# Kernel tuning notes

Measured on AMD Instinct MI355X. Metric: run time of the kernel, lower is better.

Reference implementation:

```python
import math
import jax, jax.numpy as jnp
import numpy as np

B, C_IN, H, W = 16, 384, 64, 64
CDIM, K, NSCALES, ITERS = 128, 64, 2, 3

def conv1x1(x, w, b):
    # x: [B,C,H,W], w: [O,C], b: [O]
    return jnp.einsum('bchw,oc->bohw', x, w) + b[None, :, None, None]

def mlp2(x, w1, b1, w2, b2):
    return conv1x1(jax.nn.relu(conv1x1(x, w1, b1)), w2, b2)

def log_optimal_transport(scores, dustbin, iters):
    B_, K_, N_ = scores.shape
    Z = jnp.concatenate([scores, dustbin], axis=1)  # [B,K+1,N]
    log_mu = jnp.full((B_, K_ + 1), -math.log(K_ + 1), dtype=scores.dtype)
    log_nu = jnp.full((B_, N_), -math.log(N_), dtype=scores.dtype)
    u = jnp.zeros_like(log_mu)
    v = jnp.zeros_like(log_nu)
    for _ in range(iters):
        u = log_mu - jax.nn.logsumexp(Z + v[:, None, :], axis=2)
        v = log_nu - jax.nn.logsumexp(Z + u[:, :, None], axis=1)
    return Z + u[:, :, None] + v[:, None, :]

def avg_pool2(x):
    b, c, h, w = x.shape
    return x.reshape(b, c, h // 2, 2, w // 2, 2).mean(axis=(3, 5))

def scale_branch(xs, fw1, fb1, fw2, fb2, sw1, sb1, sw2, sb2, dw1, db1, dw2, db2):
    b = xs.shape[0]
    local_feat = mlp2(xs, fw1, fb1, fw2, fb2).reshape(b, CDIM, -1)   # [B,C,N]
    score = mlp2(xs, sw1, sb1, sw2, sb2).reshape(b, K, -1)           # [B,K,N]
    dustbin = mlp2(xs, dw1, db1, dw2, db2).reshape(b, 1, -1)         # [B,1,N]
    log_p = log_optimal_transport(score, dustbin, ITERS)
    p = jnp.exp(log_p)[:, :-1, :]                                    # drop dustbin row
    p = p / (p.sum(axis=-1, keepdims=True) + 1e-8)
    out = jnp.einsum('bcn,bkn->bck', local_feat, p)                  # [B,C,K]
    out = out / jnp.clip(jnp.linalg.norm(out, axis=1, keepdims=True), 1e-12)
    return out.reshape(b, -1), local_feat

def setup_inputs():
    key = jax.random.key(0)
    ks = jax.random.split(key, 13)
    inp = {'x': jax.random.normal(ks[0], (B, C_IN, H, W), jnp.float32)}
    kidx = 1
    for s in range(NSCALES):
        for name, (o, i) in [('fw1', (512, C_IN)), ('fw2', (CDIM, 512)),
                              ('sw1', (512, C_IN)), ('sw2', (K, 512)),
                              ('dw1', (128, C_IN)), ('dw2', (1, 128))]:
            inp[f'{name}_{s}'] = 0.02 * jax.random.normal(ks[kidx % 13], (o, i), jnp.float32)
            inp[f'{name[0]}b{name[2]}_{s}'] = jnp.zeros((o,), jnp.float32)
            kidx += 1
    return inp

def reference(x,
              fw1_0, fb1_0, fw2_0, fb2_0, sw1_0, sb1_0, sw2_0, sb2_0, dw1_0, db1_0, dw2_0, db2_0,
              fw1_1, fb1_1, fw2_1, fb2_1, sw1_1, sb1_1, sw2_1, sb2_1, dw1_1, db1_1, dw2_1, db2_1):
    params = [
        (fw1_0, fb1_0, fw2_0, fb2_0, sw1_0, sb1_0, sw2_0, sb2_0, dw1_0, db1_0, dw2_0, db2_0),
        (fw1_1, fb1_1, fw2_1, fb2_1, sw1_1, sb1_1, sw2_1, sb2_1, dw1_1, db1_1, dw2_1, db2_1),
    ]
    descs = []
    xs = x
    for s in range(NSCALES):
        if s > 0:
            xs = avg_pool2(xs)
        d, _ = scale_branch(xs, *params[s])
        descs.append(d)
    g = jnp.stack(descs, axis=1).mean(axis=1)
    g = g / jnp.clip(jnp.linalg.norm(g, axis=1, keepdims=True), 1e-12)
    return g
```

## Files before the change

kernel.cpp:

```cpp
#include <hip/hip_runtime.h>
#include <math.h>

typedef __attribute__((ext_vector_type(8))) short short8;
typedef __attribute__((ext_vector_type(4))) float floatx4;

__device__ inline float bf2f(short s) {
    union { unsigned u; float f; } x; x.u = ((unsigned)(unsigned short)s) << 16; return x.f;
}
__device__ inline short f2bf(float f) {
    union { float f; unsigned u; } x; x.f = f;
    unsigned r = x.u + 0x7fff + ((x.u >> 16) & 1);
    return (short)(r >> 16);
}

struct WSet {
    const float *fw1, *fb1, *fw2, *sw1, *sb1, *sw2, *sb2, *dw1, *db1, *dw2, *db2;
};

__global__ __launch_bounds__(256) void wprep(WSet a0, WSet a1,
    short* __restrict__ W1f, short* __restrict__ W2af, short* __restrict__ W2bf,
    float* __restrict__ B1p, float* __restrict__ B2bp)
{
    const int s = blockIdx.y;
    const WSet A = s ? a1 : a0;
    W1f  += (size_t)s * 491520;
    W2af += (size_t)s * 65536;
    W2bf += (size_t)s * 98304;
    B1p  += s * 1280;
    B2bp += s * 128;
    int id = blockIdx.x * 256 + threadIdx.x;
    if (id < 491520) {
        int e = id & 7, l = (id >> 3) & 63, g = (id >> 9) & 15, rest = id >> 13;
        int kc = rest % 12, c = rest / 12;
        int m = c * 256 + g * 16 + (l & 15);
        int k = kc * 32 + (l >> 4) * 8 + e;
        float v = 0.f;
        if (m < 512) v = A.fw1[m * 384 + k];
        else if (m < 1024) v = A.sw1[(m - 512) * 384 + k];
        else if (m < 1152) v = A.dw1[(m - 1024) * 384 + k];
        W1f[id] = f2bf(v);
        return;
    }
    id -= 491520;
    if (id < 65536) {
        int e = id & 7, l = (id >> 3) & 63, g = (id >> 9) & 7, ka = id >> 12;
        int r = g * 16 + (l & 15), k = ka * 32 + (l >> 4) * 8 + e;
        W2af[id] = f2bf(A.fw2[r * 512 + k]);
        return;
    }
    id -= 65536;
    if (id < 98304) {
        int e = id & 7, l = (id >> 3) & 63, g = (id >> 9) & 7, kb = id >> 12;
        int r = g * 16 + (l & 15), krel = kb * 32 + (l >> 4) * 8 + e;
        float v = 0.f;
        if (r < 64 && krel < 512) v = A.sw2[r * 512 + krel];
        else if (r == 64 && krel >= 512 && krel < 640) v = A.dw2[krel - 512];
        W2bf[id] = f2bf(v);
        return;
    }
    id -= 98304;
    if (id < 1280) {
        float v = 0.f;
        if (id < 512) v = A.fb1[id];
        else if (id < 1024) v = A.sb1[id - 512];
        else if (id < 1152) v = A.db1[id - 1024];
        B1p[id] = v;
        return;
    }
    id -= 1280;
    if (id < 128) B2bp[id] = id < 64 ? A.sb2[id] : id == 64 ? A.db2[0] : 0.f;
}

__global__ __launch_bounds__(256) void xprep(const float* __restrict__ x,
                                             short* __restrict__ xT, short* __restrict__ x1T)
{
    __shared__ float xt[64 * 129];
    const int ip = blockIdx.x;
    const int cg = blockIdx.y;
    const int b  = blockIdx.z;
    const int t  = threadIdx.x;
    #pragma unroll
    for (int u = 0; u < 8; u++) {
        int idx = t + 256 * u;
        int c = idx >> 5, spq = idx & 31;
        float4 v = *(const float4*)&x[(((long)b * 384 + cg * 64 + c) * 64 + ip * 2 + (spq >> 4)) * 64 + (spq & 15) * 4];
        float* d = &xt[c * 129 + spq * 4];
        d[0] = v.x; d[1] = v.y; d[2] = v.z; d[3] = v.w;
    }
    __syncthreads();
    {
        int sp = t >> 1, ch = t & 1;
        short tmp[32];
        #pragma unroll
        for (int cc = 0; cc < 32; cc++) tmp[cc] = f2bf(xt[(ch * 32 + cc) * 129 + sp]);
        short* dst = xT + ((long)b * 4096 + ip * 128 + sp) * 384 + cg * 64 + ch * 32;
        #pragma unroll
        for (int v = 0; v < 4; v++) *(short8*)(dst + v * 8) = *(short8*)(tmp + v * 8);
    }
    {
        int j1 = t >> 3, c8 = t & 7;
        short tmp[8];
        #pragma unroll
        for (int e = 0; e < 8; e++) {
            int c = c8 * 8 + e;
            float v = 0.25f * (xt[c * 129 + j1 * 2]      + xt[c * 129 + j1 * 2 + 1] +
                               xt[c * 129 + 64 + j1 * 2] + xt[c * 129 + 64 + j1 * 2 + 1]);
            tmp[e] = f2bf(v);
        }
        *(short8*)(x1T + ((long)b * 1024 + ip * 32 + j1) * 384 + cg * 64 + c8 * 8) = *(short8*)tmp;
    }
}

__global__ __launch_bounds__(512, 4) void fused_mlp(
    const short* __restrict__ W1f_, const float* __restrict__ B1p_,
    const short* __restrict__ W2af_, const float* __restrict__ fb2_0, const float* __restrict__ fb2_1,
    const short* __restrict__ W2bf_, const float* __restrict__ B2bp_,
    const short* __restrict__ xT, const short* __restrict__ x1T,
    float* __restrict__ feat0, float* __restrict__ feat1,
    short* __restrict__ Eg0, short* __restrict__ Eg1,
    float* __restrict__ pu0, float* __restrict__ pu1)
{
    __shared__ short xs[12 * 2048];
    __shared__ short hs[8 * 2048];
    const int tid = threadIdx.x;
    const int wid = tid >> 6, lane = tid & 63;
    const int l15 = lane & 15, q = lane >> 4;
    const int bx = blockIdx.x, b = blockIdx.y;
    const int sc = bx >= 64;
    const int tile = sc ? bx - 64 : bx;
    const int N = sc ? 1024 : 4096;
    const int n0 = tile * 64;
    const short* XT = sc ? x1T : xT;
    const short* W1f = W1f_ + (size_t)sc * 491520;
    const float* B1p = B1p_ + sc * 1280;
    const short* W2af = W2af_ + (size_t)sc * 65536;
    const short* W2bf = W2bf_ + (size_t)sc * 98304;
    const float* fb2 = sc ? fb2_1 : fb2_0;
    const float* B2bp = B2bp_ + sc * 128;
    float* feat = (sc ? feat1 : feat0) + (long)b * 128 * N;
    short* Eg = (sc ? Eg1 : Eg0) + (long)b * 65 * N;
    float* pu = sc ? pu1 : pu0;
    const int npart = sc ? 16 : 64;

    {
        const int n = tid >> 3;
        const int c0 = (tid & 7) * 6;
        const short* src = XT + ((long)b * N + n0 + n) * 384 + c0 * 8;
        const int jj = n >> 4, nl = n & 15;
        #pragma unroll
        for (int i = 0; i < 6; i++) {
            int c = c0 + i;
            int kc = c >> 2, qq = c & 3;
            *(short8*)(xs + kc * 2048 + jj * 512 + ((qq << 4) | nl) * 8) =
                *(const short8*)(src + i * 8);
        }
    }
    __syncthreads();

    floatx4 acc2[2][4];
    #pragma unroll
    for (int i = 0; i < 2; i++)
        #pragma unroll
        for (int j = 0; j < 4; j++) acc2[i][j] = floatx4{0.f, 0.f, 0.f, 0.f};

    auto phase2 = [&](int pc) {
        if (pc < 2) {
            const short* WA = W2af + (size_t)pc * 32768;
            short8 hb[2][4], wa[2];
            #pragma unroll
            for (int j = 0; j < 4; j++) hb[0][j] = *(short8*)(hs + j * 512 + lane * 8);
            wa[0] = *(const short8*)(WA + wid * 512 + lane * 8);
            #pragma unroll
            for (int kc2 = 0; kc2 < 8; kc2++) {
                short8 bfr[4];
                #pragma unroll
                for (int j = 0; j < 4; j++) bfr[j] = hb[kc2 & 1][j];
                short8 aF = wa[kc2 & 1];
                if (kc2 + 1 < 8) {
                    #pragma unroll
                    for (int j = 0; j < 4; j++)
                        hb[(kc2 + 1) & 1][j] = *(short8*)(hs + (kc2 + 1) * 2048 + j * 512 + lane * 8);
                    wa[(kc2 + 1) & 1] = *(const short8*)(WA + ((kc2 + 1) * 8 + wid) * 512 + lane * 8);
                }
                #pragma unroll
                for (int j = 0; j < 4; j++)
                    acc2[0][j] = __builtin_amdgcn_mfma_f32_16x16x32_bf16(aF, bfr[j], acc2[0][j], 0, 0, 0);
            }
        } else {
            if (wid >= 5) return;
            const short* WB = W2bf + (size_t)(pc - 2) * 32768;
            short8 hb[2][4], we[2];
            #pragma unroll
            for (int j = 0; j < 4; j++) hb[0][j] = *(short8*)(hs + j * 512 + lane * 8);
            we[0] = *(const short8*)(WB + wid * 512 + lane * 8);
            #pragma unroll
            for (int kc2 = 0; kc2 < 8; kc2++) {
                short8 bfr[4];
                #pragma unroll
                for (int j = 0; j < 4; j++) bfr[j] = hb[kc2 & 1][j];
                short8 aE = we[kc2 & 1];
                if (kc2 + 1 < 8) {
                    #pragma unroll
                    for (int j = 0; j < 4; j++)
                        hb[(kc2 + 1) & 1][j] = *(short8*)(hs + (kc2 + 1) * 2048 + j * 512 + lane * 8);
                    we[(kc2 + 1) & 1] = *(const short8*)(WB + ((kc2 + 1) * 8 + wid) * 512 + lane * 8);
                }
                #pragma unroll
                for (int j = 0; j < 4; j++)
                    acc2[1][j] = __builtin_amdgcn_mfma_f32_16x16x32_bf16(aE, bfr[j], acc2[1][j], 0, 0, 0);
            }
        }
    };

    for (int c = 0; c < 5; c++) {
        if (c > 0) phase2(c - 1);
        floatx4 acc1[2][4];
        #pragma unroll
        for (int i = 0; i < 2; i++)
            #pragma unroll
            for (int j = 0; j < 4; j++) acc1[i][j] = floatx4{0.f, 0.f, 0.f, 0.f};
        const short* Wb = W1f + (long)c * 98304;
        short8 abuf[2][2];
        #pragma unroll
        for (int i = 0; i < 2; i++) {
            abuf[0][i] = *(const short8*)(Wb + (wid * 2 + i) * 512 + lane * 8);
            abuf[1][i] = *(const short8*)(Wb + (16 + wid * 2 + i) * 512 + lane * 8);
        }
        #pragma unroll
        for (int kc = 0; kc < 12; kc++) {
            short8 ac[2], bc[4];
            #pragma unroll
            for (int i = 0; i < 2; i++) ac[i] = abuf[kc & 1][i];
            #pragma unroll
            for (int j = 0; j < 4; j++) bc[j] = *(short8*)(xs + kc * 2048 + j * 512 + lane * 8);
            if (kc + 2 < 12) {
                #pragma unroll
                for (int i = 0; i < 2; i++)
                    abuf[kc & 1][i] = *(const short8*)(Wb + ((kc + 2) * 16 + wid * 2 + i) * 512 + lane * 8);
            }
            #pragma unroll
            for (int i = 0; i < 2; i++)
                #pragma unroll
                for (int j = 0; j < 4; j++)
                    acc1[i][j] = __builtin_amdgcn_mfma_f32_16x16x32_bf16(ac[i], bc[j], acc1[i][j], 0, 0, 0);
        }
        __syncthreads();
        #pragma unroll
        for (int i = 0; i < 2; i++) {
            const int qf = i * 2 + (q >> 1);
            const int e0 = 4 * (q & 1);
            const int mrow = c * 256 + wid * 32 + i * 16 + q * 4;
            float bw[4];
            #pragma unroll
            for (int rr = 0; rr < 4; rr++) bw[rr] = B1p[mrow + rr];
            #pragma unroll
            for (int j = 0; j < 4; j++) {
                short pk[4];
                #pragma unroll
                for (int rr = 0; rr < 4; rr++)
                    pk[rr] = f2bf(fmaxf(acc1[i][j][rr] + bw[rr], 0.f));
                *(unsigned long long*)(hs + wid * 2048 + j * 512 + ((qf << 4) | l15) * 8 + e0) =
                    *(unsigned long long*)pk;
            }
        }
        __syncthreads();
    }
    phase2(4);

    {
        const int row0 = wid * 16 + q * 4;
        #pragma unroll
        for (int rr = 0; rr < 4; rr++) {
            float bv = fb2[row0 + rr];
            #pragma unroll
            for (int j = 0; j < 4; j++)
                feat[(long)(row0 + rr) * N + n0 + 16 * j + l15] = acc2[0][j][rr] + bv;
        }
    }
    __syncthreads();
    float* puld = (float*)hs;
    if (wid < 4) {
        #pragma unroll
        for (int rr = 0; rr < 4; rr++) {
            int row = wid * 16 + q * 4 + rr;
            float bv = B2bp[row];
            float s = 0.f;
            #pragma unroll
            for (int j = 0; j < 4; j++) {
                float e = expf(acc2[1][j][rr] + bv);
                Eg[(long)row * N + n0 + 16 * j + l15] = f2bf(e);
                s += e;
            }
            s += __shfl_xor(s, 1); s += __shfl_xor(s, 2);
            s += __shfl_xor(s, 4); s += __shfl_xor(s, 8);
            if (l15 == 0) puld[row] = s;
        }
    } else if (wid == 4) {
        #pragma unroll
        for (int rr = 0; rr < 4; rr++) {
            int row = 64 + q * 4 + rr;
            bool valid = (row == 64);
            float bv = B2bp[64];
            float s = 0.f;
            #pragma unroll
            for (int j = 0; j < 4; j++) {
                float e = expf(acc2[1][j][rr] + bv);
                if (valid) {
                    Eg[(long)64 * N + n0 + 16 * j + l15] = f2bf(e);
                    s += e;
                }
            }
            s += __shfl_xor(s, 1); s += __shfl_xor(s, 2);
            s += __shfl_xor(s, 4); s += __shfl_xor(s, 8);
            if (valid && l15 == 0) puld[64] = s;
        }
    }
    __syncthreads();
    if (tid < 65)
        pu[((long)b * npart + tile) * 65 + tid] = puld[tid];
}

__global__ __launch_bounds__(256) void sk_step(
    const short* __restrict__ Eg0, const short* __restrict__ Eg1,
    const float* __restrict__ pin0, const float* __restrict__ pin1,
    float* __restrict__ pout0, float* __restrict__ pout1, int nin0, int nin1)
{
    __shared__ short Es[65 * 264];
    __shared__ float evs[256];
    __shared__ float eus[65];
    const int t = threadIdx.x;
    const int bx = blockIdx.x, b = blockIdx.y;
    const int sc = bx >= 16;
    const int chunk = sc ? bx - 16 : bx;
    const int N = sc ? 1024 : 4096;
    const float invN = sc ? (1.0f / 1024.0f) : (1.0f / 4096.0f);
    const int n0 = chunk * 256;
    const short* Eb = (sc ? Eg1 : Eg0) + (long)b * 65 * N;
    const float* pin = sc ? pin1 : pin0;
    const int nin = sc ? nin1 : nin0;
    float* pout = sc ? pout1 : pout0;
    const int nout = sc ? 4 : 16;
    if (t < 65) {
        float s = 0.f;
        for (int ch = 0; ch < nin; ch++) s += pin[((long)b * nin + ch) * 65 + t];
        eus[t] = (1.0f / 65.0f) / s;
    }
    for (int it = t; it < 2080; it += 256) {
        int k = it >> 5, n8 = it & 31;
        *(short8*)(Es + k * 264 + n8 * 8) = *(const short8*)(Eb + (long)k * N + n0 + n8 * 8);
    }
    __syncthreads();
    float sv = 0.f;
    #pragma unroll 4
    for (int k = 0; k < 65; k++) sv += bf2f(Es[k * 264 + t]) * eus[k];
    evs[t] = invN / sv;
    __syncthreads();
    const int wid = t >> 6, lane = t & 63;
    for (int k = wid; k < 65; k += 4) {
        const short* er = Es + k * 264 + lane * 4;
        float4 v4 = *(const float4*)&evs[lane * 4];
        float s = bf2f(er[0]) * v4.x + bf2f(er[1]) * v4.y + bf2f(er[2]) * v4.z + bf2f(er[3]) * v4.w;
        #pragma unroll
        for (int off = 32; off >= 1; off >>= 1) s += __shfl_xor(s, off);
        if (lane == 0) pout[((long)b * nout + chunk) * 65 + k] = s;
    }
}

__global__ __launch_bounds__(256) void sk_desc(
    const short* __restrict__ Eg0, const short* __restrict__ Eg1,
    const float* __restrict__ pin0, const float* __restrict__ pin1,
    const float* __restrict__ feat0, const float* __restrict__ feat1,
    float* __restrict__ part0, float* __restrict__ part1, int nin0, int nin1)
{
    __shared__ short Es[65 * 264];
    __shared__ float eus[65];
    __shared__ float evs[256];
    const int t = threadIdx.x;
    const int bx = blockIdx.x, b = blockIdx.y;
    const int sc = bx >= 16;
    const int chunk = sc ? bx - 16 : bx;
    const int N = sc ? 1024 : 4096;
    const float invN = sc ? (1.0f / 1024.0f) : (1.0f / 4096.0f);
    const int nch = sc ? 4 : 16;
    const int n0 = chunk * 256;
    const short* Eb = (sc ? Eg1 : Eg0) + (long)b * 65 * N;
    const float* pin = sc ? pin1 : pin0;
    const int nin = sc ? nin1 : nin0;
    const float* fb = (sc ? feat1 : feat0) + (long)b * 128 * N;
    float* part = sc ? part1 : part0;
    if (t < 65) {
        float s = 0.f;
        for (int ch = 0; ch < nin; ch++) s += pin[((long)b * nin + ch) * 65 + t];
        eus[t] = (1.0f / 65.0f) / s;
    }
    for (int it = t; it < 2080; it += 256) {
        int k = it >> 5, n8 = it & 31;
        *(short8*)(Es + k * 264 + n8 * 8) = *(const short8*)(Eb + (long)k * N + n0 + n8 * 8);
    }
    __syncthreads();
    float sv = 0.f;
    #pragma unroll 4
    for (int k = 0; k < 65; k++) sv += bf2f(Es[k * 264 + t]) * eus[k];
    evs[t] = invN / sv;
    __syncthreads();
    const int wid = t >> 6, lane = t & 63;
    const int l15 = lane & 15, q = lane >> 4;
    float* pb = part + ((long)b * nch + chunk) * 8256;
    for (int k = wid; k < 64; k += 4) {
        const short* er = Es + k * 264 + lane * 4;
        float4 v4 = *(const float4*)&evs[lane * 4];
        float s = bf2f(er[0]) * v4.x + bf2f(er[1]) * v4.y + bf2f(er[2]) * v4.z + bf2f(er[3]) * v4.w;
        #pragma unroll
        for (int off = 32; off >= 1; off >>= 1) s += __shfl_xor(s, off);
        if (lane == 0) pb[8192 + k] = s * eus[k];
    }
    floatx4 acc[2][4];
    #pragma unroll
    for (int mt = 0; mt < 2; mt++)
        #pragma unroll
        for (int nt = 0; nt < 4; nt++) acc[mt][nt] = floatx4{0.f, 0.f, 0.f, 0.f};
    #pragma unroll 2
    for (int ks = 0; ks < 8; ks++) {
        float4 ev0 = *(const float4*)&evs[ks * 32 + q * 8];
        float4 ev1 = *(const float4*)&evs[ks * 32 + q * 8 + 4];
        float evq[8] = {ev0.x, ev0.y, ev0.z, ev0.w, ev1.x, ev1.y, ev1.z, ev1.w};
        short8 ah[2], al[2];
        #pragma unroll
        for (int mt = 0; mt < 2; mt++) {
            const float* fp = fb + (long)(wid * 32 + mt * 16 + l15) * N + n0 + ks * 32 + q * 8;
            float4 v0 = *(const float4*)fp;
            float4 v1 = *(const float4*)(fp + 4);
            float va[8] = {v0.x, v0.y, v0.z, v0.w, v1.x, v1.y, v1.z, v1.w};
            short hh[8], ll[8];
            #pragma unroll
            for (int e = 0; e < 8; e++) {
                float sv2 = va[e] * evq[e];
                short h = f2bf(sv2);
                hh[e] = h;
                ll[e] = f2bf(sv2 - bf2f(h));
            }
            ah[mt] = *(short8*)hh;
            al[mt] = *(short8*)ll;
        }
        #pragma unroll
        for (int nt = 0; nt < 4; nt++) {
            short8 bfr = *(short8*)(Es + (nt * 16 + l15) * 264 + ks * 32 + q * 8);
            #pragma unroll
            for (int mt = 0; mt < 2; mt++) {
                acc[mt][nt] = __builtin_amdgcn_mfma_f32_16x16x32_bf16(al[mt], bfr, acc[mt][nt], 0, 0, 0);
                acc[mt][nt] = __builtin_amdgcn_mfma_f32_16x16x32_bf16(ah[mt], bfr, acc[mt][nt], 0, 0, 0);
            }
        }
    }
    #pragma unroll
    for (int nt = 0; nt < 4; nt++) {
        float euk = eus[nt * 16 + l15];
        #pragma unroll
        for (int mt = 0; mt < 2; mt++)
            #pragma unroll
            for (int rr = 0; rr < 4; rr++)
                pb[(wid * 32 + mt * 16 + q * 4 + rr) * 64 + nt * 16 + l15] = acc[mt][nt][rr] * euk;
    }
}

__global__ __launch_bounds__(1024) void dred_final(
    const float* __restrict__ part0, const float* __restrict__ part1,
    float* __restrict__ out, int b0)
{
    __shared__ float d0s[128 * 65];
    __shared__ float d1s[128 * 65];
    __shared__ float colp[16][64];
    __shared__ float rsv[64];
    __shared__ float red[16];
    const int b = blockIdx.x;
    const int t = threadIdx.x;
    const int c = t >> 3;
    const int k0 = (t & 7) * 8;
    const int wv = t >> 6, l = t & 63;

    #pragma unroll
    for (int s = 0; s < 2; s++) {
        const int nch = s ? 4 : 16;
        const float* pb = (s ? part1 : part0) + (long)b * nch * 8256;
        float* ds = s ? d1s : d0s;
        if (t < 64) {
            float rs = 0.f;
            for (int ch = 0; ch < nch; ch++) rs += pb[ch * 8256 + 8192 + t];
            rsv[t] = 1.0f / (rs + 1e-8f);
        }
        __syncthreads();
        float a[8];
        #pragma unroll
        for (int j = 0; j < 8; j++) a[j] = 0.f;
        for (int ch = 0; ch < nch; ch++) {
            const float* p = pb + ch * 8256 + c * 64 + k0;
            #pragma unroll
            for (int j = 0; j < 8; j++) a[j] += p[j];
        }
        #pragma unroll
        for (int j = 0; j < 8; j++) a[j] *= rsv[k0 + j];
        float v[8];
        #pragma unroll
        for (int j = 0; j < 8; j++) v[j] = a[j] * a[j];
        #pragma unroll
        for (int off = 8; off <= 32; off <<= 1)
            #pragma unroll
            for (int j = 0; j < 8; j++) v[j] += __shfl_xor(v[j], off);
        if (l < 8) {
            #pragma unroll
            for (int j = 0; j < 8; j++) colp[wv][l * 8 + j] = v[j];
        }
        __syncthreads();
        if (t < 64) {
            float sq = 0.f;
            #pragma unroll
            for (int w2 = 0; w2 < 16; w2++) sq += colp[w2][t];
            rsv[t] = 1.0f / fmaxf(sqrtf(sq), 1e-12f);
        }
        __syncthreads();
        #pragma unroll
        for (int j = 0; j < 8; j++) ds[c * 65 + k0 + j] = a[j] * rsv[k0 + j];
        __syncthreads();
    }
    float g[8];
    float ssum = 0.f;
    #pragma unroll
    for (int j = 0; j < 8; j++) {
        float v2 = (d0s[c * 65 + k0 + j] + d1s[c * 65 + k0 + j]) * 0.5f;
        g[j] = v2; ssum += v2 * v2;
    }
    #pragma unroll
    for (int off = 32; off >= 1; off >>= 1) ssum += __shfl_xor(ssum, off);
    if (l == 0) red[wv] = ssum;
    __syncthreads();
    float tot = 0.f;
    #pragma unroll
    for (int w2 = 0; w2 < 16; w2++) tot += red[w2];
    float inv = 1.0f / fmaxf(sqrtf(tot), 1e-12f);
    float* o = out + (long)(b0 + b) * 8192 + c * 64 + k0;
    #pragma unroll
    for (int j = 0; j < 8; j++) o[j] = g[j] * inv;
}

extern "C" void kernel_launch(void* const* d_in, const int* in_sizes, int n_in,
                              void* d_out, int out_size, void* d_ws, size_t ws_size,
                              hipStream_t stream)
{
    (void)in_sizes; (void)n_in; (void)out_size;
    const float* x = (const float*)d_in[0];
    WSet ws2[2];
    const float* fb2p[2];
    for (int s = 0; s < 2; s++) {
        int o = 1 + s * 12;
        ws2[s].fw1 = (const float*)d_in[o + 0];  ws2[s].fb1 = (const float*)d_in[o + 1];
        ws2[s].fw2 = (const float*)d_in[o + 2];  fb2p[s]    = (const float*)d_in[o + 3];
        ws2[s].sw1 = (const float*)d_in[o + 4];  ws2[s].sb1 = (const float*)d_in[o + 5];
        ws2[s].sw2 = (const float*)d_in[o + 6];  ws2[s].sb2 = (const float*)d_in[o + 7];
        ws2[s].dw1 = (const float*)d_in[o + 8];  ws2[s].db1 = (const float*)d_in[o + 9];
        ws2[s].dw2 = (const float*)d_in[o + 10]; ws2[s].db2 = (const float*)d_in[o + 11];
    }

    const size_t fixed = ((size_t)2*491520*2 + 2*65536*2 + 2*98304*2
                        + 2*1280*4 + 2*128*4) + (1 << 16);
    const size_t perb = (size_t)4096*384*2 + (size_t)1024*384*2
                      + (size_t)128*4096*4 + (size_t)128*1024*4
                      + (size_t)65*4096*2 + (size_t)65*1024*2
                      + (size_t)(64+16)*65*4 + (size_t)(16+4)*65*4
                      + (size_t)16*8256*4 + (size_t)4*8256*4 + 8192;
    int CB = 4;
    const int cand[3] = {16, 8, 4};
    for (int ci = 0; ci < 3; ci++)
        if (fixed + (size_t)cand[ci] * perb <= ws_size) { CB = cand[ci]; break; }

    char* p = (char*)d_ws;
    auto alloc = [&](size_t bytes) -> char* {
        char* r = p; p += (bytes + 255) & ~(size_t)255; return r;
    };
    short* W1f   = (short*)alloc((size_t)2 * 491520 * 2);
    short* W2af  = (short*)alloc((size_t)2 * 65536 * 2);
    short* W2bf  = (short*)alloc((size_t)2 * 98304 * 2);
    float* B1p   = (float*)alloc((size_t)2 * 1280 * 4);
    float* B2bp  = (float*)alloc((size_t)2 * 128 * 4);
    short* xT    = (short*)alloc((size_t)CB * 4096 * 384 * 2);
    short* x1T   = (short*)alloc((size_t)CB * 1024 * 384 * 2);
    float* feat0 = (float*)alloc((size_t)CB * 128 * 4096 * 4);
    float* feat1 = (float*)alloc((size_t)CB * 128 * 1024 * 4);
    short* Eg0   = (short*)alloc((size_t)CB * 65 * 4096 * 2);
    short* Eg1   = (short*)alloc((size_t)CB * 65 * 1024 * 2);
    float* puA0  = (float*)alloc((size_t)CB * 64 * 65 * 4);
    float* puA1  = (float*)alloc((size_t)CB * 16 * 65 * 4);
    float* puB0  = (float*)alloc((size_t)CB * 16 * 65 * 4);
    float* puB1  = (float*)alloc((size_t)CB * 4 * 65 * 4);
    float* part0 = (float*)alloc((size_t)CB * 16 * 8256 * 4);
    float* part1 = (float*)alloc((size_t)CB * 4 * 8256 * 4);

    wprep<<<dim3(2566, 2), 256, 0, stream>>>(ws2[0], ws2[1], W1f, W2af, W2bf, B1p, B2bp);
    for (int b0 = 0; b0 < 16; b0 += CB) {
        xprep<<<dim3(32, 6, CB), 256, 0, stream>>>(x + (size_t)b0 * 384 * 4096, xT, x1T);
        fused_mlp<<<dim3(80, CB), 512, 0, stream>>>(
            W1f, B1p, W2af, fb2p[0], fb2p[1], W2bf, B2bp,
            xT, x1T, feat0, feat1, Eg0, Eg1, puA0, puA1);
        sk_step<<<dim3(20, CB), 256, 0, stream>>>(Eg0, Eg1, puA0, puA1, puB0, puB1, 64, 16);
        sk_step<<<dim3(20, CB), 256, 0, stream>>>(Eg0, Eg1, puB0, puB1, puA0, puA1, 16, 4);
        sk_desc<<<dim3(20, CB), 256, 0, stream>>>(Eg0, Eg1, puA0, puA1,
                                                  feat0, feat1, part0, part1, 16, 4);
        dred_final<<<dim3(CB), 1024, 0, stream>>>(part0, part1, (float*)d_out, b0);
    }
}
```

Measured before the change: 398.4 us.

## Halve Sinkhorn chunk size, use packed bf16 converts, alias partials onto input buffers

The Sinkhorn step and descriptor kernels now process 128-column chunks instead of 256, doubling the grid to 40 blocks per batch to spread the small post-MLP stages over more CUs. Partial-sum buffers grow to match, and the descriptor partials now reuse the xT/x1T staging buffers, which shrinks the workspace so larger batch chunks may fit. Scalar bf16 rounding in xprep and the MLP epilogue is replaced with the hardware packed convert instruction. Half of each block's threads now sit idle in the column-sum phase, and dred_final has to reduce twice as many partials.

```diff
diff --git a/kernel.cpp b/kernel.cpp
--- a/kernel.cpp
+++ b/kernel.cpp
@@ -11,6 +11,11 @@
     union { float f; unsigned u; } x; x.f = f;
     unsigned r = x.u + 0x7fff + ((x.u >> 16) & 1);
     return (short)(r >> 16);
+}
+__device__ inline unsigned cvtpk2(float a, float b) {
+    unsigned r;
+    asm("v_cvt_pk_bf16_f32 %0, %1, %2" : "=v"(r) : "v"(a), "v"(b));
+    return r;
 }
 
 struct WSet {
@@ -90,22 +95,25 @@
     __syncthreads();
     {
         int sp = t >> 1, ch = t & 1;
-        short tmp[32];
-        #pragma unroll
-        for (int cc = 0; cc < 32; cc++) tmp[cc] = f2bf(xt[(ch * 32 + cc) * 129 + sp]);
+        unsigned tmp[16];
+        #pragma unroll
+        for (int cc = 0; cc < 16; cc++)
+            tmp[cc] = cvtpk2(xt[(ch * 32 + 2 * cc) * 129 + sp], xt[(ch * 32 + 2 * cc + 1) * 129 + sp]);
         short* dst = xT + ((long)b * 4096 + ip * 128 + sp) * 384 + cg * 64 + ch * 32;
         #pragma unroll
-        for (int v = 0; v < 4; v++) *(short8*)(dst + v * 8) = *(short8*)(tmp + v * 8);
+        for (int v = 0; v < 4; v++) *(short8*)(dst + v * 8) = *(short8*)(tmp + v * 4);
     }
     {
         int j1 = t >> 3, c8 = t & 7;
-        short tmp[8];
-        #pragma unroll
-        for (int e = 0; e < 8; e++) {
-            int c = c8 * 8 + e;
-            float v = 0.25f * (xt[c * 129 + j1 * 2]      + xt[c * 129 + j1 * 2 + 1] +
-                               xt[c * 129 + 64 + j1 * 2] + xt[c * 129 + 64 + j1 * 2 + 1]);
-            tmp[e] = f2bf(v);
+        unsigned tmp[4];
+        #pragma unroll
+        for (int e = 0; e < 4; e++) {
+            int c = c8 * 8 + 2 * e;
+            float v0 = 0.25f * (xt[c * 129 + j1 * 2]      + xt[c * 129 + j1 * 2 + 1] +
+                                xt[c * 129 + 64 + j1 * 2] + xt[c * 129 + 64 + j1 * 2 + 1]);
+            float v1 = 0.25f * (xt[(c + 1) * 129 + j1 * 2]      + xt[(c + 1) * 129 + j1 * 2 + 1] +
+                                xt[(c + 1) * 129 + 64 + j1 * 2] + xt[(c + 1) * 129 + 64 + j1 * 2 + 1]);
+            tmp[e] = cvtpk2(v0, v1);
         }
         *(short8*)(x1T + ((long)b * 1024 + ip * 32 + j1) * 384 + cg * 64 + c8 * 8) = *(short8*)tmp;
     }
@@ -255,12 +263,13 @@
             for (int rr = 0; rr < 4; rr++) bw[rr] = B1p[mrow + rr];
             #pragma unroll
             for (int j = 0; j < 4; j++) {
-                short pk[4];
-                #pragma unroll
-                for (int rr = 0; rr < 4; rr++)
-                    pk[rr] = f2bf(fmaxf(acc1[i][j][rr] + bw[rr], 0.f));
-                *(unsigned long long*)(hs + wid * 2048 + j * 512 + ((qf << 4) | l15) * 8 + e0) =
-                    *(unsigned long long*)pk;
+                float r0 = fmaxf(acc1[i][j][0] + bw[0], 0.f);
+                float r1 = fmaxf(acc1[i][j][1] + bw[1], 0.f);
+                float r2 = fmaxf(acc1[i][j][2] + bw[2], 0.f);
+                float r3 = fmaxf(acc1[i][j][3] + bw[3], 0.f);
+                unsigned lo = cvtpk2(r0, r1), hi = cvtpk2(r2, r3);
+                unsigned long long pk = ((unsigned long long)hi << 32) | lo;
+                *(unsigned long long*)(hs + wid * 2048 + j * 512 + ((qf << 4) | l15) * 8 + e0) = pk;
             }
         }
         __syncthreads();
@@ -325,41 +334,43 @@
     const float* __restrict__ pin0, const float* __restrict__ pin1,
     float* __restrict__ pout0, float* __restrict__ pout1, int nin0, int nin1)
 {
-    __shared__ short Es[65 * 264];
-    __shared__ float evs[256];
+    __shared__ short Es[65 * 136];
+    __shared__ float evs[128];
     __shared__ float eus[65];
     const int t = threadIdx.x;
     const int bx = blockIdx.x, b = blockIdx.y;
-    const int sc = bx >= 16;
-    const int chunk = sc ? bx - 16 : bx;
+    const int sc = bx >= 32;
+    const int chunk = sc ? bx - 32 : bx;
     const int N = sc ? 1024 : 4096;
     const float invN = sc ? (1.0f / 1024.0f) : (1.0f / 4096.0f);
-    const int n0 = chunk * 256;
+    const int n0 = chunk * 128;
     const short* Eb = (sc ? Eg1 : Eg0) + (long)b * 65 * N;
     const float* pin = sc ? pin1 : pin0;
     const int nin = sc ? nin1 : nin0;
     float* pout = sc ? pout1 : pout0;
-    const int nout = sc ? 4 : 16;
+    const int nout = sc ? 8 : 32;
     if (t < 65) {
         float s = 0.f;
         for (int ch = 0; ch < nin; ch++) s += pin[((long)b * nin + ch) * 65 + t];
         eus[t] = (1.0f / 65.0f) / s;
     }
-    for (int it = t; it < 2080; it += 256) {
-        int k = it >> 5, n8 = it & 31;
-        *(short8*)(Es + k * 264 + n8 * 8) = *(const short8*)(Eb + (long)k * N + n0 + n8 * 8);
-    }
-    __syncthreads();
-    float sv = 0.f;
-    #pragma unroll 4
-    for (int k = 0; k < 65; k++) sv += bf2f(Es[k * 264 + t]) * eus[k];
-    evs[t] = invN / sv;
+    for (int it = t; it < 1040; it += 256) {
+        int k = it >> 4, n8 = it & 15;
+        *(short8*)(Es + k * 136 + n8 * 8) = *(const short8*)(Eb + (long)k * N + n0 + n8 * 8);
+    }
+    __syncthreads();
+    if (t < 128) {
+        float sv = 0.f;
+        #pragma unroll 4
+        for (int k = 0; k < 65; k++) sv += bf2f(Es[k * 136 + t]) * eus[k];
+        evs[t] = invN / sv;
+    }
     __syncthreads();
     const int wid = t >> 6, lane = t & 63;
     for (int k = wid; k < 65; k += 4) {
-        const short* er = Es + k * 264 + lane * 4;
-        float4 v4 = *(const float4*)&evs[lane * 4];
-        float s = bf2f(er[0]) * v4.x + bf2f(er[1]) * v4.y + bf2f(er[2]) * v4.z + bf2f(er[3]) * v4.w;
+        const short* er = Es + k * 136 + lane * 2;
+        float2 v2 = *(const float2*)&evs[lane * 2];
+        float s = bf2f(er[0]) * v2.x + bf2f(er[1]) * v2.y;
         #pragma unroll
         for (int off = 32; off >= 1; off >>= 1) s += __shfl_xor(s, off);
         if (lane == 0) pout[((long)b * nout + chunk) * 65 + k] = s;
@@ -372,17 +383,17 @@
     const float* __restrict__ feat0, const float* __restrict__ feat1,
     float* __restrict__ part0, float* __restrict__ part1, int nin0, int nin1)
 {
-    __shared__ short Es[65 * 264];
+    __shared__ short Es[65 * 136];
     __shared__ float eus[65];
-    __shared__ float evs[256];
+    __shared__ float evs[128];
     const int t = threadIdx.x;
     const int bx = blockIdx.x, b = blockIdx.y;
-    const int sc = bx >= 16;
-    const int chunk = sc ? bx - 16 : bx;
+    const int sc = bx >= 32;
+    const int chunk = sc ? bx - 32 : bx;
     const int N = sc ? 1024 : 4096;
     const float invN = sc ? (1.0f / 1024.0f) : (1.0f / 4096.0f);
-    const int nch = sc ? 4 : 16;
-    const int n0 = chunk * 256;
+    const int nch = sc ? 8 : 32;
+    const int n0 = chunk * 128;
     const short* Eb = (sc ? Eg1 : Eg0) + (long)b * 65 * N;
     const float* pin = sc ? pin1 : pin0;
     const int nin = sc ? nin1 : nin0;
@@ -393,23 +404,25 @@
         for (int ch = 0; ch < nin; ch++) s += pin[((long)b * nin + ch) * 65 + t];
         eus[t] = (1.0f / 65.0f) / s;
     }
-    for (int it = t; it < 2080; it += 256) {
-        int k = it >> 5, n8 = it & 31;
-        *(short8*)(Es + k * 264 + n8 * 8) = *(const short8*)(Eb + (long)k * N + n0 + n8 * 8);
-    }
-    __syncthreads();
-    float sv = 0.f;
-    #pragma unroll 4
-    for (int k = 0; k < 65; k++) sv += bf2f(Es[k * 264 + t]) * eus[k];
-    evs[t] = invN / sv;
+    for (int it = t; it < 1040; it += 256) {
+        int k = it >> 4, n8 = it & 15;
+        *(short8*)(Es + k * 136 + n8 * 8) = *(const short8*)(Eb + (long)k * N + n0 + n8 * 8);
+    }
+    __syncthreads();
+    if (t < 128) {
+        float sv = 0.f;
+        #pragma unroll 4
+        for (int k = 0; k < 65; k++) sv += bf2f(Es[k * 136 + t]) * eus[k];
+        evs[t] = invN / sv;
+    }
     __syncthreads();
     const int wid = t >> 6, lane = t & 63;
     const int l15 = lane & 15, q = lane >> 4;
     float* pb = part + ((long)b * nch + chunk) * 8256;
     for (int k = wid; k < 64; k += 4) {
-        const short* er = Es + k * 264 + lane * 4;
-        float4 v4 = *(const float4*)&evs[lane * 4];
-        float s = bf2f(er[0]) * v4.x + bf2f(er[1]) * v4.y + bf2f(er[2]) * v4.z + bf2f(er[3]) * v4.w;
+        const short* er = Es + k * 136 + lane * 2;
+        float2 v2 = *(const float2*)&evs[lane * 2];
+        float s = bf2f(er[0]) * v2.x + bf2f(er[1]) * v2.y;
         #pragma unroll
         for (int off = 32; off >= 1; off >>= 1) s += __shfl_xor(s, off);
         if (lane == 0) pb[8192 + k] = s * eus[k];
@@ -419,8 +432,8 @@
     for (int mt = 0; mt < 2; mt++)
         #pragma unroll
         for (int nt = 0; nt < 4; nt++) acc[mt][nt] = floatx4{0.f, 0.f, 0.f, 0.f};
-    #pragma unroll 2
-    for (int ks = 0; ks < 8; ks++) {
+    #pragma unroll
+    for (int ks = 0; ks < 4; ks++) {
         float4 ev0 = *(const float4*)&evs[ks * 32 + q * 8];
         float4 ev1 = *(const float4*)&evs[ks * 32 + q * 8 + 4];
         float evq[8] = {ev0.x, ev0.y, ev0.z, ev0.w, ev1.x, ev1.y, ev1.z, ev1.w};
@@ -444,7 +457,7 @@
         }
         #pragma unroll
         for (int nt = 0; nt < 4; nt++) {
-            short8 bfr = *(short8*)(Es + (nt * 16 + l15) * 264 + ks * 32 + q * 8);
+            short8 bfr = *(short8*)(Es + (nt * 16 + l15) * 136 + ks * 32 + q * 8);
             #pragma unroll
             for (int mt = 0; mt < 2; mt++) {
                 acc[mt][nt] = __builtin_amdgcn_mfma_f32_16x16x32_bf16(al[mt], bfr, acc[mt][nt], 0, 0, 0);
@@ -480,7 +493,7 @@
 
     #pragma unroll
     for (int s = 0; s < 2; s++) {
-        const int nch = s ? 4 : 16;
+        const int nch = s ? 8 : 32;
         const float* pb = (s ? part1 : part0) + (long)b * nch * 8256;
         float* ds = s ? d1s : d0s;
         if (t < 64) {
@@ -565,8 +578,7 @@
     const size_t perb = (size_t)4096*384*2 + (size_t)1024*384*2
                       + (size_t)128*4096*4 + (size_t)128*1024*4
                       + (size_t)65*4096*2 + (size_t)65*1024*2
-                      + (size_t)(64+16)*65*4 + (size_t)(16+4)*65*4
-                      + (size_t)16*8256*4 + (size_t)4*8256*4 + 8192;
+                      + (size_t)(64+16)*65*4 + (size_t)(32+8)*65*4 + 8192;
     int CB = 4;
     const int cand[3] = {16, 8, 4};
     for (int ci = 0; ci < 3; ci++)
@@ -589,10 +601,10 @@
     short* Eg1   = (short*)alloc((size_t)CB * 65 * 1024 * 2);
     float* puA0  = (float*)alloc((size_t)CB * 64 * 65 * 4);
     float* puA1  = (float*)alloc((size_t)CB * 16 * 65 * 4);
-    float* puB0  = (float*)alloc((size_t)CB * 16 * 65 * 4);
-    float* puB1  = (float*)alloc((size_t)CB * 4 * 65 * 4);
-    float* part0 = (float*)alloc((size_t)CB * 16 * 8256 * 4);
-    float* part1 = (float*)alloc((size_t)CB * 4 * 8256 * 4);
+    float* puB0  = (float*)alloc((size_t)CB * 32 * 65 * 4);
+    float* puB1  = (float*)alloc((size_t)CB * 8 * 65 * 4);
+    float* part0 = (float*)xT;
+    float* part1 = (float*)x1T;
 
     wprep<<<dim3(2566, 2), 256, 0, stream>>>(ws2[0], ws2[1], W1f, W2af, W2bf, B1p, B2bp);
     for (int b0 = 0; b0 < 16; b0 += CB) {
@@ -600,10 +612,10 @@
         fused_mlp<<<dim3(80, CB), 512, 0, stream>>>(
             W1f, B1p, W2af, fb2p[0], fb2p[1], W2bf, B2bp,
             xT, x1T, feat0, feat1, Eg0, Eg1, puA0, puA1);
-        sk_step<<<dim3(20, CB), 256, 0, stream>>>(Eg0, Eg1, puA0, puA1, puB0, puB1, 64, 16);
-        sk_step<<<dim3(20, CB), 256, 0, stream>>>(Eg0, Eg1, puB0, puB1, puA0, puA1, 16, 4);
-        sk_desc<<<dim3(20, CB), 256, 0, stream>>>(Eg0, Eg1, puA0, puA1,
-                                                  feat0, feat1, part0, part1, 16, 4);
+        sk_step<<<dim3(40, CB), 256, 0, stream>>>(Eg0, Eg1, puA0, puA1, puB0, puB1, 64, 16);
+        sk_step<<<dim3(40, CB), 256, 0, stream>>>(Eg0, Eg1, puB0, puB1, puA0, puA1, 32, 8);
+        sk_desc<<<dim3(40, CB), 256, 0, stream>>>(Eg0, Eg1, puA0, puA1,
+                                                  feat0, feat1, part0, part1, 32, 8);
         dred_final<<<dim3(CB), 1024, 0, stream>>>(part0, part1, (float*)d_out, b0);
     }
 }
```

Result: no change. 396.0 us (-0.6%).
